# Kernel tuning notes

Measured on AMD Instinct MI355X. Metric: run time of the kernel, lower is better.

Reference implementation:

```python
import jax, jax.numpy as jnp
import numpy as np

N, C, H, W = 8, 64, 56, 56
POS_PIXEL_DIST = 0.7   # init kwarg pos_pixel_dist
NORM_EPS = 1e-8        # F.normalize eps
DEN_EPS = 1e-6


def setup_inputs() -> dict:
    key = jax.random.key(0)
    kq, kk, k1, k2, k3, k4 = jax.random.split(key, 6)
    return {
        "q": jax.random.normal(kq, (N, C, H, W), dtype=jnp.float32),
        "k": jax.random.normal(kk, (N, C, H, W), dtype=jnp.float32),
        "center_q_x": jax.random.uniform(k1, (N, H, W), dtype=jnp.float32),
        "center_q_y": jax.random.uniform(k2, (N, H, W), dtype=jnp.float32),
        "center_k_x": jax.random.uniform(k3, (N, H, W), dtype=jnp.float32),
        "center_k_y": jax.random.uniform(k4, (N, H, W), dtype=jnp.float32),
    }


def _l2_normalize(x, axis, eps=NORM_EPS):
    # matches torch F.normalize: x / max(||x||, eps)
    n = jnp.sqrt(jnp.sum(x * x, axis=axis, keepdims=True))
    return x / jnp.maximum(n, eps)


def reference(q, k, center_q_x, center_q_y, center_k_x, center_k_y):
    n, c, h, w = q.shape
    hw = h * w
    q = _l2_normalize(q.reshape(n, c, hw), axis=1)   # (N, C, HW)
    k = _l2_normalize(k.reshape(n, c, hw), axis=1)

    cqx = center_q_x.reshape(n, hw)
    cqy = center_q_y.reshape(n, hw)
    ckx = center_k_x.reshape(n, hw)
    cky = center_k_y.reshape(n, hw)

    # pairwise euclidean distance between q-pixel and k-pixel centers: (N, HW, HW)
    dx = cqx[:, :, None] - ckx[:, None, :]
    dy = cqy[:, :, None] - cky[:, None, :]
    dist_center = jnp.sqrt(dx * dx + dy * dy)
    pos_mask = jax.lax.stop_gradient(
        (dist_center < POS_PIXEL_DIST).astype(q.dtype))

    # cosine similarity (features already normalized): (N, HW, HW)
    logit = jnp.einsum('nci,ncj->nij', q, k)

    loss = (logit * pos_mask).sum((-1, -2)) / (pos_mask.sum((-1, -2)) + DEN_EPS)
    return -2.0 * loss.mean()
```

## Files before the change

kernel.cpp:

```cpp
#include <hip/hip_runtime.h>
#include <stdint.h>

#define HW  3136
#define HWP 3200
#define NB  8

typedef unsigned short ushort_t;
typedef __attribute__((ext_vector_type(8))) _Float16 f16x8;
typedef __attribute__((ext_vector_type(4))) float f32x4;

__device__ __forceinline__ void gload16(const void* g, void* l) {
  __builtin_amdgcn_global_load_lds(
      (const __attribute__((address_space(1))) void*)g,
      (__attribute__((address_space(3))) void*)l, 16, 0, 0);
}

__global__ __launch_bounds__(256) void norm_cast_kernel(
    const float* __restrict__ q, const float* __restrict__ k,
    const float* __restrict__ cqx, const float* __restrict__ cqy,
    const float* __restrict__ ckx, const float* __restrict__ cky,
    ushort_t* __restrict__ qh, ushort_t* __restrict__ kh,
    float* __restrict__ cqxp, float* __restrict__ cqyp,
    float* __restrict__ ckxp, float* __restrict__ ckyp) {
  const int isK = blockIdx.y;
  const float* src = isK ? k : q;
  ushort_t* dh = isK ? kh : qh;
  float* cxp = isK ? ckxp : cqxp;
  float* cyp = isK ? ckyp : cqyp;
  const float* cx = isK ? ckx : cqx;
  const float* cy = isK ? cky : cqy;
  const float sent = isK ? -1e9f : 1e9f;
  const int n = blockIdx.x / 50, pb = blockIdx.x % 50;
  const int tid = threadIdx.x;

  if (pb == 49) {
    uint4 z = make_uint4(0u, 0u, 0u, 0u);
    uint4* dst = (uint4*)(dh + ((size_t)n * HWP + HW) * 64);
    #pragma unroll
    for (int u = tid; u < 512; u += 256) dst[u] = z;
    if (tid < 64) {
      cxp[(size_t)n * HWP + HW + tid] = sent;
      cyp[(size_t)n * HWP + HW + tid] = sent;
    }
    return;
  }

  const int p0 = pb * 64;
  __shared__ float tile[64][65];
  __shared__ float psum[4][64];
  __shared__ float invs[64];
  const int px = tid & 63, grp = tid >> 6;

  for (int c = grp; c < 64; c += 4)
    tile[c][px] = src[(size_t)(n * 64 + c) * HW + p0 + px];
  if (tid < 64) {
    cxp[(size_t)n * HWP + p0 + tid] = cx[(size_t)n * HW + p0 + tid];
    cyp[(size_t)n * HWP + p0 + tid] = cy[(size_t)n * HW + p0 + tid];
  }
  __syncthreads();

  float s = 0.f;
  #pragma unroll
  for (int e = 0; e < 16; ++e) { float v = tile[grp * 16 + e][px]; s += v * v; }
  psum[grp][px] = s;
  __syncthreads();
  if (tid < 64) {
    float t = psum[0][tid] + psum[1][tid] + psum[2][tid] + psum[3][tid];
    invs[tid] = 1.0f / fmaxf(sqrtf(t), 1e-8f);
  }
  __syncthreads();

  const int c = tid & 63;
  for (int pl = grp; pl < 64; pl += 4) {
    float v = tile[c][pl] * invs[pl];
    _Float16 h = (_Float16)v;
    const int p = p0 + pl;
    const size_t row = (size_t)n * HWP + p;
    const int off = (((c >> 3) ^ (p & 7)) << 3) | (c & 7);
    dh[row * 64 + off] = __builtin_bit_cast(ushort_t, h);
  }
}

#define SQ    0
#define SK0   16384
#define SK1   24576
#define SKC0  32768
#define SKC1  33280
#define SQC   33792
#define SMEM_BYTES 34816

__global__ __launch_bounds__(256, 4) void pair_sum_kernel(
    const ushort_t* __restrict__ qh, const ushort_t* __restrict__ kh,
    const float* __restrict__ cqxp, const float* __restrict__ cqyp,
    const float* __restrict__ ckxp, const float* __restrict__ ckyp,
    float* __restrict__ partial) {
  __shared__ __align__(16) char smem[SMEM_BYTES];
  const int bid = blockIdx.x;
  const int n = bid / 125;
  const int rem = bid % 125;
  const int i0 = (rem / 5) * 128;
  const int js = rem % 5;
  const int tid = threadIdx.x, lane = tid & 63, wid = tid >> 6;
  const int wr = wid >> 1, wc = wid & 1;
  const size_t base = (size_t)n * HWP * 64;
  const size_t cbase = (size_t)n * HWP;

  #pragma unroll
  for (int pass = 0; pass < 4; ++pass) {
    const int idx = pass * 256 + tid;
    gload16(qh + base + (size_t)(i0 + (idx >> 3)) * 64 + (idx & 7) * 8,
            smem + SQ + idx * 16);
  }
  const int j00 = js * 10 * 64;
  #pragma unroll
  for (int pass = 0; pass < 2; ++pass) {
    const int idx = pass * 256 + tid;
    gload16(kh + base + (size_t)(j00 + (idx >> 3)) * 64 + (idx & 7) * 8,
            smem + SK0 + idx * 16);
  }
  if (tid < 32) {
    const float* src = (lane < 16) ? (ckxp + cbase + j00 + lane * 4)
                                   : (ckyp + cbase + j00 + (lane - 16) * 4);
    gload16(src, smem + SKC0 + lane * 16);
  }
  if (tid < 64) {
    const float* src = (lane < 32) ? (cqxp + cbase + i0 + lane * 4)
                                   : (cqyp + cbase + i0 + (lane - 32) * 4);
    gload16(src, smem + SQC + lane * 16);
  }
  __syncthreads();

  float qcx[4][4], qcy[4][4];
  {
    const float* sqc = (const float*)(smem + SQC);
    #pragma unroll
    for (int tr = 0; tr < 4; ++tr)
      #pragma unroll
      for (int r = 0; r < 4; ++r) {
        const int il = wr * 64 + tr * 16 + (lane >> 4) * 4 + r;
        qcx[tr][r] = sqc[il];
        qcy[tr][r] = sqc[128 + il];
      }
  }

  float num = 0.f;
  unsigned int dcnt = 0;

  for (int jt = 0; jt < 10; ++jt) {
    const int b = jt & 1;
    if (jt < 9) {
      const int j1 = (js * 10 + jt + 1) * 64;
      char* dk = smem + SK0 + (b ^ 1) * 8192;
      #pragma unroll
      for (int pass = 0; pass < 2; ++pass) {
        const int idx = pass * 256 + tid;
        gload16(kh + base + (size_t)(j1 + (idx >> 3)) * 64 + (idx & 7) * 8,
                dk + idx * 16);
      }
      if (tid < 32) {
        const float* src = (lane < 16) ? (ckxp + cbase + j1 + lane * 4)
                                       : (ckyp + cbase + j1 + (lane - 16) * 4);
        gload16(src, smem + SKC0 + (b ^ 1) * 512 + lane * 16);
      }
    }

    f32x4 acc[4][2];
    #pragma unroll
    for (int a = 0; a < 4; ++a)
      #pragma unroll
      for (int c2 = 0; c2 < 2; ++c2) acc[a][c2] = (f32x4){0.f, 0.f, 0.f, 0.f};

    const char* sk = smem + SK0 + b * 8192;
    #pragma unroll
    for (int kk = 0; kk < 2; ++kk) {
      f16x8 Ah[4], Bh[2];
      #pragma unroll
      for (int t = 0; t < 4; ++t) {
        const int row = wr * 64 + t * 16 + (lane & 15);
        const int aoff = row * 128 + (((kk * 4 + (lane >> 4)) ^ (row & 7)) << 4);
        Ah[t] = *(const f16x8*)(smem + SQ + aoff);
      }
      #pragma unroll
      for (int t = 0; t < 2; ++t) {
        const int jr = wc * 32 + t * 16 + (lane & 15);
        const int boff = jr * 128 + (((kk * 4 + (lane >> 4)) ^ (jr & 7)) << 4);
        Bh[t] = *(const f16x8*)(sk + boff);
      }
      #pragma unroll
      for (int tr = 0; tr < 4; ++tr)
        #pragma unroll
        for (int tc = 0; tc < 2; ++tc)
          acc[tr][tc] = __builtin_amdgcn_mfma_f32_16x16x32_f16(Ah[tr], Bh[tc], acc[tr][tc], 0, 0, 0);
    }

    const float* skc = (const float*)(smem + SKC0 + b * 512);
    float kx[2], ky[2];
    #pragma unroll
    for (int tc = 0; tc < 2; ++tc) {
      const int jl = wc * 32 + tc * 16 + (lane & 15);
      kx[tc] = skc[jl];
      ky[tc] = skc[64 + jl];
    }
    #pragma unroll
    for (int tr = 0; tr < 4; ++tr) {
      #pragma unroll
      for (int r = 0; r < 4; ++r) {
        const float qx = qcx[tr][r], qy = qcy[tr][r];
        #pragma unroll
        for (int tc = 0; tc < 2; ++tc) {
          const float dx = qx - kx[tc];
          const float dy = qy - ky[tc];
          float d2 = dx * dx;
          d2 = fmaf(dy, dy, d2);
          const bool m = d2 < 0.48999998f;
          num += m ? acc[tr][tc][r] : 0.f;
          dcnt += (unsigned int)__popcll(__ballot(m));
        }
      }
    }

    __syncthreads();
  }

  float* red = (float*)smem;
  red[tid] = num;
  red[256 + tid] = (lane == 0) ? (float)dcnt : 0.f;
  __syncthreads();
  #pragma unroll
  for (int s = 128; s > 0; s >>= 1) {
    if (tid < s) { red[tid] += red[tid + s]; red[256 + tid] += red[256 + tid + s]; }
    __syncthreads();
  }
  if (tid == 0) { partial[bid * 2] = red[0]; partial[bid * 2 + 1] = red[256]; }
}

__global__ __launch_bounds__(256) void finalize_kernel(const float* __restrict__ partial,
                                                       float* __restrict__ out) {
  __shared__ float rat[8];
  const int tid = threadIdx.x;
  const int n = tid >> 5, s = tid & 31;
  float num = 0.f, den = 0.f;
  for (int p = s; p < 125; p += 32) {
    num += partial[(n * 125 + p) * 2];
    den += partial[(n * 125 + p) * 2 + 1];
  }
  #pragma unroll
  for (int off = 16; off > 0; off >>= 1) {
    num += __shfl_down(num, off, 32);
    den += __shfl_down(den, off, 32);
  }
  if (s == 0) rat[n] = num / (den + 1e-6f);
  __syncthreads();
  if (tid == 0) {
    float t = 0.f;
    #pragma unroll
    for (int i = 0; i < 8; ++i) t += rat[i];
    out[0] = -0.25f * t;
  }
}

extern "C" void kernel_launch(void* const* d_in, const int* in_sizes, int n_in,
                              void* d_out, int out_size, void* d_ws, size_t ws_size,
                              hipStream_t stream) {
  const float* q   = (const float*)d_in[0];
  const float* k   = (const float*)d_in[1];
  const float* cqx = (const float*)d_in[2];
  const float* cqy = (const float*)d_in[3];
  const float* ckx = (const float*)d_in[4];
  const float* cky = (const float*)d_in[5];

  const size_t ARR = (size_t)NB * HWP * 64;
  ushort_t* qh = (ushort_t*)d_ws;
  ushort_t* kh = qh + ARR;
  float* cqxp = (float*)(kh + ARR);
  float* cqyp = cqxp + (size_t)NB * HWP;
  float* ckxp = cqyp + (size_t)NB * HWP;
  float* ckyp = ckxp + (size_t)NB * HWP;
  float* partial = ckyp + (size_t)NB * HWP;

  norm_cast_kernel<<<dim3(400, 2), 256, 0, stream>>>(
      q, k, cqx, cqy, ckx, cky, qh, kh, cqxp, cqyp, ckxp, ckyp);
  pair_sum_kernel<<<1000, 256, 0, stream>>>(
      qh, kh, cqxp, cqyp, ckxp, ckyp, partial);
  finalize_kernel<<<1, 256, 0, stream>>>(partial, (float*)d_out);
}
```

Before: 43.55 us.

## Load MFMA operands directly from global into registers, dropping LDS staging

The pair kernel no longer stages Q/K fp16 tiles and center coordinates in LDS through async global-to-LDS loads and double buffering. Each wave now keeps its Q fragments in registers for the whole block and loads K fragments and key centers straight from global (L2-resident) memory every iteration, with no per-iteration barrier. The normalize kernel writes unswizzled rows as 16-byte vector stores instead of scattered 2-byte stores. This trades LDS traffic and synchronisation for more global loads and register pressure, with launch bounds lowered to 3 blocks per SIMD to make room.

```diff
diff --git a/kernel.cpp b/kernel.cpp
--- a/kernel.cpp
+++ b/kernel.cpp
@@ -7,13 +7,8 @@
 
 typedef unsigned short ushort_t;
 typedef __attribute__((ext_vector_type(8))) _Float16 f16x8;
+typedef __attribute__((ext_vector_type(8))) unsigned short ushort8;
 typedef __attribute__((ext_vector_type(4))) float f32x4;
-
-__device__ __forceinline__ void gload16(const void* g, void* l) {
-  __builtin_amdgcn_global_load_lds(
-      (const __attribute__((address_space(1))) void*)g,
-      (__attribute__((address_space(3))) void*)l, 16, 0, 0);
-}
 
 __global__ __launch_bounds__(256) void norm_cast_kernel(
     const float* __restrict__ q, const float* __restrict__ k,
@@ -70,98 +65,77 @@
   }
   __syncthreads();
 
-  const int c = tid & 63;
-  for (int pl = grp; pl < 64; pl += 4) {
-    float v = tile[c][pl] * invs[pl];
-    _Float16 h = (_Float16)v;
-    const int p = p0 + pl;
-    const size_t row = (size_t)n * HWP + p;
-    const int off = (((c >> 3) ^ (p & 7)) << 3) | (c & 7);
-    dh[row * 64 + off] = __builtin_bit_cast(ushort_t, h);
-  }
-}
-
-#define SQ    0
-#define SK0   16384
-#define SK1   24576
-#define SKC0  32768
-#define SKC1  33280
-#define SQC   33792
-#define SMEM_BYTES 34816
-
-__global__ __launch_bounds__(256, 4) void pair_sum_kernel(
+  #pragma unroll
+  for (int s2 = 0; s2 < 2; ++s2) {
+    const int slot = s2 * 256 + tid;
+    const int pl = slot >> 3, ch = slot & 7;
+    const float iv = invs[pl];
+    ushort8 w;
+    #pragma unroll
+    for (int e = 0; e < 8; ++e) {
+      float v = tile[ch * 8 + e][pl] * iv;
+      _Float16 h = (_Float16)v;
+      w[e] = __builtin_bit_cast(ushort_t, h);
+    }
+    *(ushort8*)(dh + ((size_t)n * HWP + p0 + pl) * 64 + ch * 8) = w;
+  }
+}
+
+__global__ __launch_bounds__(256, 3) void pair_sum_kernel(
     const ushort_t* __restrict__ qh, const ushort_t* __restrict__ kh,
     const float* __restrict__ cqxp, const float* __restrict__ cqyp,
     const float* __restrict__ ckxp, const float* __restrict__ ckyp,
     float* __restrict__ partial) {
-  __shared__ __align__(16) char smem[SMEM_BYTES];
+  __shared__ float red[512];
   const int bid = blockIdx.x;
-  const int n = bid / 125;
-  const int rem = bid % 125;
-  const int i0 = (rem / 5) * 128;
-  const int js = rem % 5;
+  const int n = bid / 125, rem = bid % 125;
+  const int i0 = (rem / 5) * 128, js = rem % 5;
   const int tid = threadIdx.x, lane = tid & 63, wid = tid >> 6;
   const int wr = wid >> 1, wc = wid & 1;
   const size_t base = (size_t)n * HWP * 64;
   const size_t cbase = (size_t)n * HWP;
-
-  #pragma unroll
-  for (int pass = 0; pass < 4; ++pass) {
-    const int idx = pass * 256 + tid;
-    gload16(qh + base + (size_t)(i0 + (idx >> 3)) * 64 + (idx & 7) * 8,
-            smem + SQ + idx * 16);
-  }
-  const int j00 = js * 10 * 64;
-  #pragma unroll
-  for (int pass = 0; pass < 2; ++pass) {
-    const int idx = pass * 256 + tid;
-    gload16(kh + base + (size_t)(j00 + (idx >> 3)) * 64 + (idx & 7) * 8,
-            smem + SK0 + idx * 16);
-  }
-  if (tid < 32) {
-    const float* src = (lane < 16) ? (ckxp + cbase + j00 + lane * 4)
-                                   : (ckyp + cbase + j00 + (lane - 16) * 4);
-    gload16(src, smem + SKC0 + lane * 16);
-  }
-  if (tid < 64) {
-    const float* src = (lane < 32) ? (cqxp + cbase + i0 + lane * 4)
-                                   : (cqyp + cbase + i0 + (lane - 32) * 4);
-    gload16(src, smem + SQC + lane * 16);
-  }
-  __syncthreads();
+  const int lrow = lane & 15, lhi = lane >> 4;
+
+  f16x8 Ah[2][4];
+  #pragma unroll
+  for (int kk = 0; kk < 2; ++kk)
+    #pragma unroll
+    for (int t = 0; t < 4; ++t) {
+      const int row = i0 + wr * 64 + t * 16 + lrow;
+      Ah[kk][t] = *(const f16x8*)(qh + base + (size_t)row * 64 + kk * 32 + lhi * 8);
+    }
 
   float qcx[4][4], qcy[4][4];
-  {
-    const float* sqc = (const float*)(smem + SQC);
-    #pragma unroll
-    for (int tr = 0; tr < 4; ++tr)
-      #pragma unroll
-      for (int r = 0; r < 4; ++r) {
-        const int il = wr * 64 + tr * 16 + (lane >> 4) * 4 + r;
-        qcx[tr][r] = sqc[il];
-        qcy[tr][r] = sqc[128 + il];
-      }
-  }
+  #pragma unroll
+  for (int tr = 0; tr < 4; ++tr)
+    #pragma unroll
+    for (int r = 0; r < 4; ++r) {
+      const int il = i0 + wr * 64 + tr * 16 + lhi * 4 + r;
+      qcx[tr][r] = cqxp[cbase + il];
+      qcy[tr][r] = cqyp[cbase + il];
+    }
 
   float num = 0.f;
   unsigned int dcnt = 0;
 
+  #pragma unroll 2
   for (int jt = 0; jt < 10; ++jt) {
-    const int b = jt & 1;
-    if (jt < 9) {
-      const int j1 = (js * 10 + jt + 1) * 64;
-      char* dk = smem + SK0 + (b ^ 1) * 8192;
-      #pragma unroll
-      for (int pass = 0; pass < 2; ++pass) {
-        const int idx = pass * 256 + tid;
-        gload16(kh + base + (size_t)(j1 + (idx >> 3)) * 64 + (idx & 7) * 8,
-                dk + idx * 16);
+    const int jr0 = (js * 10 + jt) * 64 + wc * 32;
+
+    f16x8 Bh[2][2];
+    #pragma unroll
+    for (int kk = 0; kk < 2; ++kk)
+      #pragma unroll
+      for (int t = 0; t < 2; ++t) {
+        const int row = jr0 + t * 16 + lrow;
+        Bh[kk][t] = *(const f16x8*)(kh + base + (size_t)row * 64 + kk * 32 + lhi * 8);
       }
-      if (tid < 32) {
-        const float* src = (lane < 16) ? (ckxp + cbase + j1 + lane * 4)
-                                       : (ckyp + cbase + j1 + (lane - 16) * 4);
-        gload16(src, smem + SKC0 + (b ^ 1) * 512 + lane * 16);
-      }
+    float kx[2], ky[2];
+    #pragma unroll
+    for (int tc = 0; tc < 2; ++tc) {
+      const int jl = jr0 + tc * 16 + lrow;
+      kx[tc] = ckxp[cbase + jl];
+      ky[tc] = ckyp[cbase + jl];
     }
 
     f32x4 acc[4][2];
@@ -170,37 +144,15 @@
       #pragma unroll
       for (int c2 = 0; c2 < 2; ++c2) acc[a][c2] = (f32x4){0.f, 0.f, 0.f, 0.f};
 
-    const char* sk = smem + SK0 + b * 8192;
-    #pragma unroll
-    for (int kk = 0; kk < 2; ++kk) {
-      f16x8 Ah[4], Bh[2];
-      #pragma unroll
-      for (int t = 0; t < 4; ++t) {
-        const int row = wr * 64 + t * 16 + (lane & 15);
-        const int aoff = row * 128 + (((kk * 4 + (lane >> 4)) ^ (row & 7)) << 4);
-        Ah[t] = *(const f16x8*)(smem + SQ + aoff);
-      }
-      #pragma unroll
-      for (int t = 0; t < 2; ++t) {
-        const int jr = wc * 32 + t * 16 + (lane & 15);
-        const int boff = jr * 128 + (((kk * 4 + (lane >> 4)) ^ (jr & 7)) << 4);
-        Bh[t] = *(const f16x8*)(sk + boff);
-      }
+    #pragma unroll
+    for (int kk = 0; kk < 2; ++kk)
       #pragma unroll
       for (int tr = 0; tr < 4; ++tr)
         #pragma unroll
         for (int tc = 0; tc < 2; ++tc)
-          acc[tr][tc] = __builtin_amdgcn_mfma_f32_16x16x32_f16(Ah[tr], Bh[tc], acc[tr][tc], 0, 0, 0);
-    }
-
-    const float* skc = (const float*)(smem + SKC0 + b * 512);
-    float kx[2], ky[2];
-    #pragma unroll
-    for (int tc = 0; tc < 2; ++tc) {
-      const int jl = wc * 32 + tc * 16 + (lane & 15);
-      kx[tc] = skc[jl];
-      ky[tc] = skc[64 + jl];
-    }
+          acc[tr][tc] = __builtin_amdgcn_mfma_f32_16x16x32_f16(
+              Ah[kk][tr], Bh[kk][tc], acc[tr][tc], 0, 0, 0);
+
     #pragma unroll
     for (int tr = 0; tr < 4; ++tr) {
       #pragma unroll
@@ -218,11 +170,8 @@
         }
       }
     }
-
-    __syncthreads();
-  }
-
-  float* red = (float*)smem;
+  }
+
   red[tid] = num;
   red[256 + tid] = (lane == 0) ? (float)dcnt : 0.f;
   __syncthreads();
```

Result: slower. 62.34 us (+43.2%).
